# Kernel optimization log

Measured on AMD Instinct MI355X. Metric: run time of the kernel, lower is better.

## Reference

```python
import jax, jax.numpy as jnp
import numpy as np

EPS = 1e-5

def setup_inputs() -> dict:
    key = jax.random.key(0)
    ks = jax.random.split(key, 4)
    B, F, H, W = 32, 2048, 7, 7
    hw = H * W
    A = 1
    return {
        "x": jax.random.normal(ks[0], (B, F, H, W), dtype=jnp.float32),
        "W_qkv": jax.random.normal(ks[1], (3 * hw, hw), dtype=jnp.float32) * (hw ** -0.5),
        "W_out": jax.random.normal(ks[2], (A, hw), dtype=jnp.float32) * (hw ** -0.5),
        "b_out": jax.random.normal(ks[3], (A,), dtype=jnp.float32) * 0.01,
        "gamma": jnp.ones((F,), dtype=jnp.float32),
        "beta": jnp.zeros((F,), dtype=jnp.float32),
    }

def reference(x, W_qkv, W_out, b_out, gamma, beta):
    B, F, H, W = x.shape
    hw = H * W
    scale = hw ** -0.5
    xf = x.reshape(B, F, hw)                       # [B, F, 49]
    qkv = jnp.einsum("bfd,ed->bfe", xf, W_qkv)   # [B, F, 147]
    q, k, v = jnp.split(qkv, 3, axis=-1)           # each [B, F, 49]
    scores = jnp.einsum("bfd,bgd->bfg", q, k) * scale   # [B, F, F]
    probs = jax.nn.softmax(scores, axis=-1)
    attn_out = jnp.einsum("bfg,bgd->bfd", probs, v)      # [B, F, 49]
    out = jnp.einsum("bfd,ad->bfa", attn_out, W_out) + b_out  # [B, F, A]
    # BatchNorm1d (training mode): per-channel (axis=1) stats over (batch, length)
    mean = out.mean(axis=(0, 2), keepdims=True)
    var = out.var(axis=(0, 2), keepdims=True)  # biased variance, as torch uses for normalization
    out = (out - mean) * jax.lax.rsqrt(var + EPS)
    return out * gamma[None, :, None] + beta[None, :, None]
```

## Files before the change

### kernel.cpp

```cpp
#include <hip/hip_runtime.h>
#include <math.h>

#define BB    32
#define FF    2048
#define HW    49
#define ROWS  (BB * FF)
#define DPAD  64
#define SPLIT 4
#define GHALF (FF / SPLIT)
#define NST   (GHALF / 32)

typedef float f32x16 __attribute__((ext_vector_type(16)));
typedef _Float16 f16x8 __attribute__((ext_vector_type(8)));
typedef short s16x8 __attribute__((ext_vector_type(8)));

__device__ inline float exp2_fast(float x) {
    return __builtin_amdgcn_exp2f(x);
}

__device__ inline unsigned f16pack(float v) {
    _Float16 h = (_Float16)v;
    _Float16 l = (_Float16)(v - (float)h);
    unsigned hb = (unsigned)__builtin_bit_cast(unsigned short, h);
    unsigned lb = (unsigned)__builtin_bit_cast(unsigned short, l);
    return (hb << 16) | lb;
}

__device__ inline void unpack8(uint4 a, uint4 b, f16x8& h, f16x8& l) {
    unsigned w[8] = {a.x, a.y, a.z, a.w, b.x, b.y, b.z, b.w};
    s16x8 hs, ls;
    #pragma unroll
    for (int i = 0; i < 8; ++i) {
        hs[i] = (short)(w[i] >> 16);
        ls[i] = (short)(w[i] & 0xFFFFu);
    }
    h = __builtin_bit_cast(f16x8, hs);
    l = __builtin_bit_cast(f16x8, ls);
}

__global__ __launch_bounds__(256) void prep_kernel(
    const float* __restrict__ Wqkv, const float* __restrict__ Wout,
    unsigned* __restrict__ Mtpk, float* __restrict__ u)
{
    __shared__ float W2[98][52];
    const int tid = threadIdx.x;
    if (blockIdx.x < 16) {
        for (int i = tid; i < 98 * 52; i += 256) {
            int e = i / 52, j = i - e * 52;
            W2[e][j] = (j < HW) ? Wqkv[e * HW + j] : 0.f;
        }
        __syncthreads();
        const int d = blockIdx.x * 4 + (tid >> 6);
        const int j = tid & 63;
        float s = 0.f;
        if (d < HW && j < HW) {
            for (int e = 0; e < HW; ++e) s = fmaf(W2[e][j], W2[49 + e][d], s);
            s *= 0.2060992915555662f;
        }
        Mtpk[d * 64 + j] = f16pack(s);
    } else {
        if (tid < 64) {
            float s = 0.f;
            if (tid < HW)
                for (int e = 0; e < HW; ++e)
                    s = fmaf(Wqkv[(98 + e) * HW + tid], Wout[e], s);
            u[tid] = s;
        }
    }
}

__global__ __launch_bounds__(256) void xy_kernel(
    const float* __restrict__ x, const float* __restrict__ u,
    const unsigned* __restrict__ Mtpk,
    unsigned short* __restrict__ xf, unsigned short* __restrict__ yh,
    float* __restrict__ wv)
{
    __shared__ float xsh[128 * HW];
    __shared__ float ush[64];
    const int blk = (blockIdx.x & 7) * 64 + (blockIdx.x >> 3);
    const int tid = threadIdx.x, lane = tid & 63, wid = tid >> 6;
    const int col = lane & 31, half = lane >> 5;
    if (tid < 64) ush[tid] = u[tid];

    {
        const float* xb = x + (size_t)blk * 128 * HW;
        for (int i = tid; i < 128 * HW; i += 256) xsh[i] = xb[i];
    }
    __syncthreads();

    const int r0 = blk * 128 + wid * 32;
    const int rloc = wid * 32 + col;
    const int row = r0 + col;
    const int tile = blk * 4 + wid;

    f16x8 ah[4], al[4];
    float wp = 0.f;
    #pragma unroll
    for (int ks = 0; ks < 4; ++ks) {
        s16x8 hs, ls;
        #pragma unroll
        for (int i = 0; i < 8; ++i) {
            int d = ks * 16 + half * 8 + i;
            float t = (d < HW) ? xsh[rloc * HW + d] : 0.f;
            wp = fmaf(t, ush[d], wp);
            _Float16 h = (_Float16)t;
            _Float16 l = (_Float16)(t - (float)h);
            hs[i] = __builtin_bit_cast(short, h);
            ls[i] = __builtin_bit_cast(short, l);
        }
        ah[ks] = __builtin_bit_cast(f16x8, hs);
        al[ks] = __builtin_bit_cast(f16x8, ls);
        *(f16x8*)(xf + ((size_t)tile * 4 + ks) * 512 + lane * 8) = ah[ks];
    }
    wp += __shfl_xor(wp, 32);
    if (half == 0) wv[row] = wp;

    for (int dt = 0; dt < 2; ++dt) {
        f16x8 mh[4], ml[4];
        #pragma unroll
        for (int ks = 0; ks < 4; ++ks) {
            const unsigned* mp = Mtpk + (dt * 32 + col) * 64 + ks * 16 + half * 8;
            unpack8(*(const uint4*)mp, *(const uint4*)(mp + 4), mh[ks], ml[ks]);
        }
        f32x16 acc;
        #pragma unroll
        for (int i = 0; i < 16; ++i) acc[i] = 0.f;
        #pragma unroll
        for (int ks = 0; ks < 4; ++ks) {
            acc = __builtin_amdgcn_mfma_f32_32x32x16_f16(ah[ks], ml[ks], acc, 0, 0, 0);
            acc = __builtin_amdgcn_mfma_f32_32x32x16_f16(al[ks], mh[ks], acc, 0, 0, 0);
            acc = __builtin_amdgcn_mfma_f32_32x32x16_f16(ah[ks], mh[ks], acc, 0, 0, 0);
        }
        #pragma unroll
        for (int reg = 0; reg < 16; ++reg) {
            int drow = (reg & 3) + 8 * (reg >> 2) + 4 * half;
            _Float16 hv = (_Float16)acc[reg];
            yh[(size_t)(r0 + drow) * DPAD + dt * 32 + col] =
                __builtin_bit_cast(unsigned short, hv);
        }
    }
}

__global__ __launch_bounds__(256, 4) void attn_kernel(
    const unsigned short* __restrict__ xf, const unsigned short* __restrict__ yh,
    const float* __restrict__ wv,
    float* __restrict__ partL, float* __restrict__ partA)
{
    const int bid = blockIdx.x;
    const int L = (bid & 7) * 256 + (bid >> 3);
    const int b   = L >> 6;
    const int r63 = L & 63;

    const int tid  = threadIdx.x;
    const int lane = tid & 63;
    const int wid  = tid >> 6;
    const int col  = lane & 31;
    const int half = lane >> 5;

    const int sp  = r63 >> 4;
    const int ftg = (r63 & 15) * 4 + wid;
    const int fblk0  = ftg * 32;
    const int gstart = sp * GHALF;
    const size_t bq = (size_t)b * FF;

    f16x8 qhf[4];
    {
        const size_t yrow = (bq + fblk0 + col) * DPAD;
        #pragma unroll
        for (int ks = 0; ks < 4; ++ks)
            qhf[ks] = *(const f16x8*)(yh + yrow + ks * 16 + half * 8);
    }

    const unsigned short* abase =
        xf + ((size_t)(b * (FF / 32) + sp * NST) * 4) * 512 + lane * 8;
    const float* wbase = wv + bq + gstart + 4 * half;

    float lsum = 0.f;
    float a0 = 0.f, a1 = 0.f, a2 = 0.f, a3 = 0.f;

    f16x8 af[3][4];
    #pragma unroll
    for (int ks = 0; ks < 4; ++ks)
        af[0][ks] = *(const f16x8*)(abase + (size_t)ks * 512);
    #pragma unroll
    for (int ks = 0; ks < 4; ++ks)
        af[1][ks] = *(const f16x8*)(abase + (size_t)2048 + ks * 512);

    #pragma unroll
    for (int t = 0; t < NST; ++t) {
        if (t + 2 < NST) {
            #pragma unroll
            for (int ks = 0; ks < 4; ++ks)
                af[(t + 2) % 3][ks] =
                    *(const f16x8*)(abase + (size_t)(t + 2) * 2048 + ks * 512);
        }

        f32x16 acc;
        #pragma unroll
        for (int i = 0; i < 16; ++i) acc[i] = 0.f;
        #pragma unroll
        for (int ks = 0; ks < 4; ++ks)
            acc = __builtin_amdgcn_mfma_f32_32x32x16_f16(af[t % 3][ks], qhf[ks],
                                                         acc, 0, 0, 0);
        const float* wpb = wbase + t * 32;
        #pragma unroll
        for (int q = 0; q < 4; ++q) {
            float4 w4 = *(const float4*)(wpb + q * 8);
            float p0 = exp2_fast(acc[q * 4 + 0]);
            float p1 = exp2_fast(acc[q * 4 + 1]);
            float p2 = exp2_fast(acc[q * 4 + 2]);
            float p3 = exp2_fast(acc[q * 4 + 3]);
            lsum += ((p0 + p1) + (p2 + p3));
            a0 = fmaf(p0, w4.x, a0);
            a1 = fmaf(p1, w4.y, a1);
            a2 = fmaf(p2, w4.z, a2);
            a3 = fmaf(p3, w4.w, a3);
        }
    }

    float asum = (a0 + a1) + (a2 + a3);
    lsum += __shfl_xor(lsum, 32);
    asum += __shfl_xor(asum, 32);
    if (half == 0) {
        size_t o = ((size_t)sp * BB + b) * FF + fblk0 + col;
        partL[o] = lsum;
        partA[o] = asum;
    }
}

__global__ __launch_bounds__(64) void bn_kernel(
    const float* __restrict__ partL, const float* __restrict__ partA,
    const float* __restrict__ gamma, const float* __restrict__ beta,
    float* __restrict__ out)
{
    const int f = blockIdx.x * 64 + threadIdx.x;
    float v[BB];
    float mean = 0.f;
    #pragma unroll
    for (int b = 0; b < BB; ++b) {
        float l = 0.f, a = 0.f;
        #pragma unroll
        for (int s = 0; s < SPLIT; ++s) {
            l += partL[((size_t)s * BB + b) * FF + f];
            a += partA[((size_t)s * BB + b) * FF + f];
        }
        v[b] = a / l;
        mean += v[b];
    }
    mean *= (1.f / BB);
    float var = 0.f;
    #pragma unroll
    for (int b = 0; b < BB; ++b) {
        float d = v[b] - mean;
        var = fmaf(d, d, var);
    }
    var *= (1.f / BB);
    const float inv = rsqrtf(var + 1e-5f);
    const float g = gamma[f], be = beta[f];
    #pragma unroll
    for (int b = 0; b < BB; ++b)
        out[((size_t)b << 11) + f] = (v[b] - mean) * inv * g + be;
}

extern "C" void kernel_launch(void* const* d_in, const int* in_sizes, int n_in,
                              void* d_out, int out_size, void* d_ws, size_t ws_size,
                              hipStream_t stream)
{
    const float* x     = (const float*)d_in[0];
    const float* Wqkv  = (const float*)d_in[1];
    const float* Wout  = (const float*)d_in[2];
    const float* gamma = (const float*)d_in[4];
    const float* beta  = (const float*)d_in[5];

    char* wsb = (char*)d_ws;
    const size_t PANEL = (size_t)ROWS * DPAD * sizeof(unsigned short);
    unsigned short* xf = (unsigned short*)(wsb);
    unsigned short* yh = (unsigned short*)(wsb + PANEL);
    float*          wv = (float*)(wsb + 2 * PANEL);
    unsigned*     Mtpk = (unsigned*)(wsb + 2 * PANEL + 262144);
    float*           u = (float*)(wsb + 2 * PANEL + 262144 + 16384);
    float*       partL = (float*)(wsb + 2 * PANEL + 262144 + 17408);
    float*       partA = partL + (size_t)SPLIT * BB * FF;

    prep_kernel<<<dim3(17), dim3(256), 0, stream>>>(Wqkv, Wout, Mtpk, u);

    xy_kernel<<<dim3(ROWS / 128), dim3(256), 0, stream>>>(
        x, u, Mtpk, xf, yh, wv);

    attn_kernel<<<dim3(BB * 64), dim3(256), 0, stream>>>(
        xf, yh, wv, partL, partA);

    bn_kernel<<<dim3(FF / 64), dim3(64), 0, stream>>>(
        partL, partA, gamma, beta, (float*)d_out);
}
```

Measured before the change: 70.26 us.

## Halve xy_kernel block size and pair two independent MFMA chains in attention loop

The xy_kernel now runs 128-thread blocks over 64 rows each, doubling the grid and halving shared memory per block so more blocks can be resident. The attention loop drops the three-deep register prefetch ring and instead processes two key tiles per iteration (tile j and tile j+HNST) with separate accumulators. This gives the scheduler two independent MFMA chains to interleave with the exp work. The loads are no longer prefetched ahead, so memory latency may be exposed more, while register pressure changes.

After: 71.80 us. 2.2% more time.

```diff
diff --git a/kernel.cpp b/kernel.cpp
--- a/kernel.cpp
+++ b/kernel.cpp
@@ -9,6 +9,7 @@
 #define SPLIT 4
 #define GHALF (FF / SPLIT)
 #define NST   (GHALF / 32)
+#define HNST  (NST / 2)
 
 typedef float f32x16 __attribute__((ext_vector_type(16)));
 typedef _Float16 f16x8 __attribute__((ext_vector_type(8)));
@@ -69,29 +70,29 @@
     }
 }
 
-__global__ __launch_bounds__(256) void xy_kernel(
+__global__ __launch_bounds__(128) void xy_kernel(
     const float* __restrict__ x, const float* __restrict__ u,
     const unsigned* __restrict__ Mtpk,
     unsigned short* __restrict__ xf, unsigned short* __restrict__ yh,
     float* __restrict__ wv)
 {
-    __shared__ float xsh[128 * HW];
+    __shared__ float xsh[64 * HW];
     __shared__ float ush[64];
-    const int blk = (blockIdx.x & 7) * 64 + (blockIdx.x >> 3);
+    const int blk = (blockIdx.x & 7) * 128 + (blockIdx.x >> 3);
     const int tid = threadIdx.x, lane = tid & 63, wid = tid >> 6;
     const int col = lane & 31, half = lane >> 5;
     if (tid < 64) ush[tid] = u[tid];
 
     {
-        const float* xb = x + (size_t)blk * 128 * HW;
-        for (int i = tid; i < 128 * HW; i += 256) xsh[i] = xb[i];
+        const float* xb = x + (size_t)blk * 64 * HW;
+        for (int i = tid; i < 64 * HW; i += 128) xsh[i] = xb[i];
     }
     __syncthreads();
 
-    const int r0 = blk * 128 + wid * 32;
+    const int r0 = blk * 64 + wid * 32;
     const int rloc = wid * 32 + col;
     const int row = r0 + col;
-    const int tile = blk * 4 + wid;
+    const int tile = blk * 2 + wid;
 
     f16x8 ah[4], al[4];
     float wp = 0.f;
@@ -178,38 +179,48 @@
     float lsum = 0.f;
     float a0 = 0.f, a1 = 0.f, a2 = 0.f, a3 = 0.f;
 
-    f16x8 af[3][4];
-    #pragma unroll
-    for (int ks = 0; ks < 4; ++ks)
-        af[0][ks] = *(const f16x8*)(abase + (size_t)ks * 512);
-    #pragma unroll
-    for (int ks = 0; ks < 4; ++ks)
-        af[1][ks] = *(const f16x8*)(abase + (size_t)2048 + ks * 512);
-
-    #pragma unroll
-    for (int t = 0; t < NST; ++t) {
-        if (t + 2 < NST) {
-            #pragma unroll
-            for (int ks = 0; ks < 4; ++ks)
-                af[(t + 2) % 3][ks] =
-                    *(const f16x8*)(abase + (size_t)(t + 2) * 2048 + ks * 512);
-        }
-
-        f32x16 acc;
-        #pragma unroll
-        for (int i = 0; i < 16; ++i) acc[i] = 0.f;
-        #pragma unroll
-        for (int ks = 0; ks < 4; ++ks)
-            acc = __builtin_amdgcn_mfma_f32_32x32x16_f16(af[t % 3][ks], qhf[ks],
-                                                         acc, 0, 0, 0);
-        const float* wpb = wbase + t * 32;
+    #pragma unroll
+    for (int j = 0; j < HNST; ++j) {
+        f16x8 af0[4], af1[4];
+        #pragma unroll
+        for (int ks = 0; ks < 4; ++ks)
+            af0[ks] = *(const f16x8*)(abase + (size_t)j * 2048 + ks * 512);
+        #pragma unroll
+        for (int ks = 0; ks < 4; ++ks)
+            af1[ks] = *(const f16x8*)(abase + (size_t)(j + HNST) * 2048 + ks * 512);
+
+        f32x16 acc0, acc1;
+        #pragma unroll
+        for (int i = 0; i < 16; ++i) { acc0[i] = 0.f; acc1[i] = 0.f; }
+        #pragma unroll
+        for (int ks = 0; ks < 4; ++ks)
+            acc0 = __builtin_amdgcn_mfma_f32_32x32x16_f16(af0[ks], qhf[ks], acc0, 0, 0, 0);
+        #pragma unroll
+        for (int ks = 0; ks < 4; ++ks)
+            acc1 = __builtin_amdgcn_mfma_f32_32x32x16_f16(af1[ks], qhf[ks], acc1, 0, 0, 0);
+
+        const float* wpb0 = wbase + j * 32;
         #pragma unroll
         for (int q = 0; q < 4; ++q) {
-            float4 w4 = *(const float4*)(wpb + q * 8);
-            float p0 = exp2_fast(acc[q * 4 + 0]);
-            float p1 = exp2_fast(acc[q * 4 + 1]);
-            float p2 = exp2_fast(acc[q * 4 + 2]);
-            float p3 = exp2_fast(acc[q * 4 + 3]);
+            float4 w4 = *(const float4*)(wpb0 + q * 8);
+            float p0 = exp2_fast(acc0[q * 4 + 0]);
+            float p1 = exp2_fast(acc0[q * 4 + 1]);
+            float p2 = exp2_fast(acc0[q * 4 + 2]);
+            float p3 = exp2_fast(acc0[q * 4 + 3]);
+            lsum += ((p0 + p1) + (p2 + p3));
+            a0 = fmaf(p0, w4.x, a0);
+            a1 = fmaf(p1, w4.y, a1);
+            a2 = fmaf(p2, w4.z, a2);
+            a3 = fmaf(p3, w4.w, a3);
+        }
+        const float* wpb1 = wbase + (j + HNST) * 32;
+        #pragma unroll
+        for (int q = 0; q < 4; ++q) {
+            float4 w4 = *(const float4*)(wpb1 + q * 8);
+            float p0 = exp2_fast(acc1[q * 4 + 0]);
+            float p1 = exp2_fast(acc1[q * 4 + 1]);
+            float p2 = exp2_fast(acc1[q * 4 + 2]);
+            float p3 = exp2_fast(acc1[q * 4 + 3]);
             lsum += ((p0 + p1) + (p2 + p3));
             a0 = fmaf(p0, w4.x, a0);
             a1 = fmaf(p1, w4.y, a1);
@@ -284,7 +295,7 @@
 
     prep_kernel<<<dim3(17), dim3(256), 0, stream>>>(Wqkv, Wout, Mtpk, u);
 
-    xy_kernel<<<dim3(ROWS / 128), dim3(256), 0, stream>>>(
+    xy_kernel<<<dim3(ROWS / 64), dim3(128), 0, stream>>>(
         x, u, Mtpk, xf, yh, wv);
 
     attn_kernel<<<dim3(BB * 64), dim3(256), 0, stream>>>(
```
